# Performance work log

Hardware: AMD Instinct MI355X
Metric: run time of the kernel (lower is better)

The kernel has to match this reference:

```python
import jax, jax.numpy as jnp
import numpy as np

N_NODES = 10000
N_EDGES = 160000
D = 42          # node_input_dim == node_hidden_dim
DE = 10         # edge_input_dim
DEH = 42        # edge_hidden_dim
N_STEPS = 6


def setup_inputs() -> dict:
    key = jax.random.key(0)
    ks = jax.random.split(key, 16)
    s = 0.1
    return {
        "n_feat": jax.random.normal(ks[0], (N_NODES, D), jnp.float32),
        "e_feat": jax.random.normal(ks[1], (N_EDGES, DE), jnp.float32),
        "src": jax.random.randint(ks[2], (N_EDGES,), 0, N_NODES),
        "dst": jax.random.randint(ks[3], (N_EDGES,), 0, N_NODES),
        # lin0: node_input_dim -> node_hidden_dim
        "lin0_w": s * jax.random.normal(ks[4], (D, D), jnp.float32),
        "lin0_b": s * jax.random.normal(ks[5], (D,), jnp.float32),
        # message_layer: hidden -> hidden
        "msg_w": s * jax.random.normal(ks[6], (D, D), jnp.float32),
        "msg_b": s * jax.random.normal(ks[7], (D,), jnp.float32),
        # edge_network: Linear(10,42) -> ReLU -> Linear(42, 42*42)
        "en_w1": s * jax.random.normal(ks[8], (DE, DEH), jnp.float32),
        "en_b1": s * jax.random.normal(ks[9], (DEH,), jnp.float32),
        "en_w2": s * jax.random.normal(ks[10], (DEH, D * D), jnp.float32),
        "en_b2": s * jax.random.normal(ks[11], (D * D,), jnp.float32),
        # NNConv bias (DGL NNConv has bias=True by default)
        "conv_b": s * jax.random.normal(ks[12], (D,), jnp.float32),
    }


def reference(n_feat, e_feat, src, dst,
              lin0_w, lin0_b, msg_w, msg_b,
              en_w1, en_b1, en_w2, en_b2, conv_b):
    N, d = n_feat.shape
    init = n_feat
    out = jax.nn.relu(n_feat @ lin0_w + lin0_b)                      # [N, d]
    # Per-edge weight matrices from edge features (e_feat is constant
    # across steps, so the edge MLP is hoisted out of the loop).
    w_edge = (jax.nn.relu(e_feat @ en_w1 + en_b1) @ en_w2 + en_b2)   # [E, d*d]
    w_edge = w_edge.reshape(-1, d, d)                                # [E, d_in, d_out]
    for _ in range(N_STEPS):
        # NNConv: gather src feats, per-edge matvec, scatter-sum to dst
        msgs = jnp.einsum('ei,eio->eo', out[src], w_edge)            # [E, d]
        agg = jax.ops.segment_sum(msgs, dst, num_segments=N)         # [N, d]
        # residual (in==out -> identity res_fc) + bias, then outer ReLU
        m = jax.nn.relu(agg + out + conv_b)
        out = jax.nn.relu(m @ msg_w + msg_b)
    return out + init
```

## Files before the change

### kernel.cpp

```cpp
#include <hip/hip_runtime.h>
#include <hip/hip_bf16.h>


#define N_NODES 10000
#define N_EDGES 160000
#define NCHK 5000
#define D 42
#define DE 10
#define XSTR 48
#define KI 1806
#define NKSTEP 57
#define SSTR 1832

typedef __attribute__((ext_vector_type(8))) short short8;
typedef __attribute__((ext_vector_type(4))) float f32x4;

__global__ __launch_bounds__(256) void k_lin0(const float* __restrict__ nf,
        const float* __restrict__ w, const float* __restrict__ b,
        __hip_bfloat16* __restrict__ out16) {
    int idx = blockIdx.x * 256 + threadIdx.x;
    if (idx >= N_NODES * XSTR) return;
    int n = idx / XSTR, j = idx % XSTR;
    float v = 0.f;
    if (j < D) {
        const float* row = nf + n * D;
        float acc = b[j];
        #pragma unroll
        for (int i = 0; i < D; ++i) acc = fmaf(row[i], w[i * D + j], acc);
        v = fmaxf(acc, 0.f);
    }
    out16[idx] = __float2bfloat16(v);
}

__global__ __launch_bounds__(256) void k_T2B(const float* __restrict__ w2,
        const float* __restrict__ b2, __hip_bfloat16* __restrict__ Bfr) {
    int idx = blockIdx.x * 256 + threadIdx.x;
    if (idx >= 3 * NKSTEP * 64 * 8) return;
    int j = idx & 7, lane = (idx >> 3) & 63;
    int ks = (idx >> 9) % NKSTEP, nt = idx / (NKSTEP * 512);
    int col = nt * 16 + (lane & 15);
    int k = ks * 32 + ((lane >> 4) * 8) + j;
    float v = 0.f;
    if (col < D && k < KI) {
        int kk = k / D, ii = k % D;
        v = (kk < D) ? w2[kk * (D * D) + ii * D + col] : b2[ii * D + col];
    }
    Bfr[idx] = __float2bfloat16(v);
}

__global__ __launch_bounds__(256) void k_hist(const int* __restrict__ dst,
        int* __restrict__ cnt) {
    int e = blockIdx.x * 256 + threadIdx.x;
    if (e < N_EDGES) atomicAdd(&cnt[dst[e]], 1);
}

__global__ __launch_bounds__(1024) void k_scan(const int* __restrict__ cnt,
        int* __restrict__ row_ptr, int* __restrict__ cursor) {
    __shared__ int buf[1024];
    __shared__ int s_run;
    const int t = threadIdx.x;
    if (t == 0) s_run = 0;
    __syncthreads();
    for (int base = 0; base < N_NODES; base += 1024) {
        int v = (base + t < N_NODES) ? cnt[base + t] : 0;
        buf[t] = v;
        __syncthreads();
        for (int off = 1; off < 1024; off <<= 1) {
            int add = (t >= off) ? buf[t - off] : 0;
            __syncthreads();
            buf[t] += add;
            __syncthreads();
        }
        int excl = buf[t] - v;
        if (base + t < N_NODES) {
            int val = s_run + excl;
            row_ptr[base + t] = val;
            cursor[base + t]  = val;
        }
        __syncthreads();
        if (t == 0) s_run += buf[1023];
        __syncthreads();
    }
    if (t == 0) { row_ptr[N_NODES] = s_run; cursor[N_NODES] = s_run; }
}

__global__ __launch_bounds__(256) void k_scatter(const int* __restrict__ dst,
        const int* __restrict__ src, int* __restrict__ cursor,
        int* __restrict__ srcp, int* __restrict__ eperm) {
    int e = blockIdx.x * 256 + threadIdx.x;
    if (e < N_EDGES) {
        int p = atomicAdd(&cursor[dst[e]], 1);
        srcp[p] = src[e];
        eperm[p] = e;
    }
}

__global__ __launch_bounds__(256) void k_hT(const float* __restrict__ ef,
        const float* __restrict__ w1, const float* __restrict__ b1,
        const int* __restrict__ eperm, __hip_bfloat16* __restrict__ hpT) {
    const int c = blockIdx.x;
    const int t = threadIdx.x;
    for (int j = t; j < 48 * 32; j += 256) {
        int k = j >> 5, ep = j & 31;
        int e = eperm[c * 32 + ep];
        float v;
        if (k < D) {
            const float* row = ef + (size_t)e * DE;
            float acc = b1[k];
            #pragma unroll
            for (int i = 0; i < DE; ++i) acc = fmaf(row[i], w1[i * D + k], acc);
            v = fmaxf(acc, 0.f);
        } else {
            v = (k == D) ? 1.0f : 0.f;
        }
        hpT[(size_t)c * 1536 + j] = __float2bfloat16(v);
    }
}

#define MFMA(A, B, C) C = __builtin_amdgcn_mfma_f32_16x16x32_bf16(A, B, C, 0, 0, 0)

__global__ __launch_bounds__(512, 6) void k_step6(
        const __hip_bfloat16* __restrict__ hpT,
        const __hip_bfloat16* __restrict__ out_in,
        const int* __restrict__ srcp, const int* __restrict__ row_ptr,
        const __hip_bfloat16* __restrict__ Bfr,
        const float* __restrict__ nf, const float* __restrict__ msg_w,
        const float* __restrict__ msg_b, const float* __restrict__ conv_b,
        __hip_bfloat16* __restrict__ out16_dst, float* __restrict__ fout,
        int last) {
    __shared__ __align__(16) __hip_bfloat16 sS[8 * SSTR];
    __shared__ float sR[8 * 48];
    __shared__ float sM[8 * 48];
    const int t = threadIdx.x;
    const int wv = t >> 6;
    const int l = t & 63;
    const int g = l >> 4;
    const int g8 = g * 8;
    const int cl = l & 15;
    const int n0 = blockIdx.x * 8;
    const short* hpTs = (const short*)hpT;
    const short* xs = (const short*)out_in;

    for (int i = t; i < 8 * 48; i += 512) sR[i] = 0.f;
    for (int i = t; i < 8 * 18; i += 512)
        sS[(i / 18) * SSTR + KI + (i % 18)] = __float2bfloat16(0.f);

    {
        const int node = n0 + wv;
        const int beg = row_ptr[node], end = row_ptr[node + 1];
        const int c0 = beg >> 5;
        const int nc = (end > beg) ? ((end - 1) >> 5) - c0 + 1 : 0;

        f32x4 cc[9];
        #pragma unroll
        for (int i = 0; i < 9; ++i) cc[i] = {0.f, 0.f, 0.f, 0.f};

        for (int ci = 0; ci < nc; ++ci) {
            const int c = c0 + ci;
            const int c32 = c << 5;
            const size_t hb = (size_t)c * 1536 + cl * 32 + g8;
            short8 a0 = *(const short8*)(hpTs + hb);
            short8 a1 = *(const short8*)(hpTs + hb + 512);
            short8 a2 = *(const short8*)(hpTs + hb + 1024);
            if (c32 < beg || c32 + 32 > end) {
                #pragma unroll
                for (int j = 0; j < 8; ++j) {
                    int ep = c32 + g8 + j;
                    if (ep < beg || ep >= end) { a0[j] = 0; a1[j] = 0; a2[j] = 0; }
                }
            }
            int4 s0 = *(const int4*)(srcp + c32 + g8);
            int4 s1 = *(const int4*)(srcp + c32 + g8 + 4);
            const int se[8] = {s0.x, s0.y, s0.z, s0.w, s1.x, s1.y, s1.z, s1.w};
            #pragma unroll
            for (int nt = 0; nt < 3; ++nt) {
                short8 b;
                #pragma unroll
                for (int j = 0; j < 8; ++j)
                    b[j] = xs[(size_t)se[j] * XSTR + nt * 16 + cl];
                MFMA(a0, b, cc[0 * 3 + nt]);
                MFMA(a1, b, cc[1 * 3 + nt]);
                MFMA(a2, b, cc[2 * 3 + nt]);
            }
        }
        #define ST(CI, MT, NT)                                               \
            _Pragma("unroll")                                                \
            for (int r = 0; r < 4; ++r) {                                    \
                int m = (MT) * 16 + g * 4 + r;                               \
                int col = (NT) * 16 + cl;                                    \
                if (m < 43 && col < D)                                       \
                    sS[wv * SSTR + m * D + col] = __float2bfloat16(cc[CI][r]); \
            }
        ST(0, 0, 0) ST(1, 0, 1) ST(2, 0, 2)
        ST(3, 1, 0) ST(4, 1, 1) ST(5, 1, 2)
        ST(6, 2, 0) ST(7, 2, 1) ST(8, 2, 2)
        #undef ST
    }
    __syncthreads();

    {
        const int ks0 = (wv == 0) ? 0 : (wv * 7 + 1);
        const int ks1 = wv * 7 + 8;
        f32x4 d0 = {0.f, 0.f, 0.f, 0.f}, d1 = d0, d2 = d0;
        const short* sSrow = (const short*)sS + (cl & 7) * SSTR + g8;
        const short* bb = (const short*)Bfr + (size_t)l * 8;
        for (int ks = ks0; ks < ks1; ++ks) {
            short8 a  = *(const short8*)(sSrow + ks * 32);
            short8 B0 = *(const short8*)(bb + (size_t)(0 * NKSTEP + ks) * 512);
            short8 B1 = *(const short8*)(bb + (size_t)(1 * NKSTEP + ks) * 512);
            short8 B2 = *(const short8*)(bb + (size_t)(2 * NKSTEP + ks) * 512);
            MFMA(a, B0, d0); MFMA(a, B1, d1); MFMA(a, B2, d2);
        }
        if (g < 2) {
            const int rl = g * 4;
            #pragma unroll
            for (int r = 0; r < 4; ++r) {
                atomicAdd(&sR[(rl + r) * 48 + cl],      d0[r]);
                atomicAdd(&sR[(rl + r) * 48 + 16 + cl], d1[r]);
                atomicAdd(&sR[(rl + r) * 48 + 32 + cl], d2[r]);
            }
        }
    }
    __syncthreads();

    float* sW = (float*)sS;
    for (int i = t; i < D * D; i += 512) sW[i] = msg_w[i];
    for (int idx = t; idx < 8 * 48; idx += 512) {
        int nl_ = idx / 48, o = idx % 48;
        float mv = 0.f;
        if (o < D) {
            float res = __bfloat162float(out_in[(size_t)(n0 + nl_) * XSTR + o]);
            mv = fmaxf(sR[idx] + res + conv_b[o], 0.f);
        }
        sM[idx] = mv;
    }
    __syncthreads();

    for (int idx = t; idx < 8 * 48; idx += 512) {
        int nl_ = idx / 48, pcol = idx % 48;
        if (pcol < D) {
            float s = msg_b[pcol];
            #pragma unroll 6
            for (int o = 0; o < D; ++o)
                s = fmaf(sM[nl_ * 48 + o], sW[o * D + pcol], s);
            float v = fmaxf(s, 0.f);
            if (last) {
                fout[(size_t)(n0 + nl_) * D + pcol] =
                    v + nf[(size_t)(n0 + nl_) * D + pcol];
            } else {
                out16_dst[(size_t)(n0 + nl_) * XSTR + pcol] = __float2bfloat16(v);
            }
        } else if (!last) {
            out16_dst[(size_t)(n0 + nl_) * XSTR + pcol] = __float2bfloat16(0.f);
        }
    }
}

extern "C" void kernel_launch(void* const* d_in, const int* in_sizes, int n_in,
                              void* d_out, int out_size, void* d_ws, size_t ws_size,
                              hipStream_t stream) {
    const float* nf    = (const float*)d_in[0];
    const float* ef    = (const float*)d_in[1];
    const int*   src   = (const int*)d_in[2];
    const int*   dst   = (const int*)d_in[3];
    const float* lin0w = (const float*)d_in[4];
    const float* lin0b = (const float*)d_in[5];
    const float* msgw  = (const float*)d_in[6];
    const float* msgb  = (const float*)d_in[7];
    const float* enw1  = (const float*)d_in[8];
    const float* enb1  = (const float*)d_in[9];
    const float* enw2  = (const float*)d_in[10];
    const float* enb2  = (const float*)d_in[11];
    const float* convb = (const float*)d_in[12];

    char* p = (char*)d_ws;
    auto alloc = [&](size_t bytes) -> char* {
        char* r = p; p += (bytes + 255) & ~(size_t)255; return r;
    };
    __hip_bfloat16* outA = (__hip_bfloat16*)alloc((size_t)N_NODES * XSTR * 2);
    __hip_bfloat16* outB = (__hip_bfloat16*)alloc((size_t)N_NODES * XSTR * 2);
    __hip_bfloat16* hpT  = (__hip_bfloat16*)alloc((size_t)NCHK * 1536 * 2);
    __hip_bfloat16* Bfr  = (__hip_bfloat16*)alloc((size_t)3 * NKSTEP * 64 * 8 * 2);
    int* cnt    = (int*)alloc((N_NODES + 1) * 4);
    int* rowp   = (int*)alloc((N_NODES + 1) * 4);
    int* cur    = (int*)alloc((N_NODES + 1) * 4);
    int* srcp   = (int*)alloc((size_t)N_EDGES * 4);
    int* eperm  = (int*)alloc((size_t)N_EDGES * 4);

    hipMemsetAsync(cnt, 0, (N_NODES + 1) * 4, stream);
    k_lin0<<<(N_NODES * XSTR + 255) / 256, 256, 0, stream>>>(nf, lin0w, lin0b, outA);
    k_T2B<<<(3 * NKSTEP * 64 * 8 + 255) / 256, 256, 0, stream>>>(enw2, enb2, Bfr);
    k_hist<<<(N_EDGES + 255) / 256, 256, 0, stream>>>(dst, cnt);
    k_scan<<<1, 1024, 0, stream>>>(cnt, rowp, cur);
    k_scatter<<<(N_EDGES + 255) / 256, 256, 0, stream>>>(dst, src, cur, srcp, eperm);
    k_hT<<<NCHK, 256, 0, stream>>>(ef, enw1, enb1, eperm, hpT);

    const int tiles = N_NODES / 8;
    __hip_bfloat16* bufs[2] = {outA, outB};
    for (int s_i = 0; s_i < 6; ++s_i) {
        const __hip_bfloat16* cin = bufs[s_i % 2];
        __hip_bfloat16* cout = bufs[(s_i + 1) % 2];
        int last = (s_i == 5) ? 1 : 0;
        k_step6<<<tiles, 512, 0, stream>>>(hpT, cin, srcp, rowp, Bfr,
                                           nf, msgw, msgb, convb,
                                           cout, (float*)d_out, last);
    }
}
```

Measured before the change: 365.9 us.

## Fuse six step launches into one persistent cooperative kernel with grid sync

```diff
diff --git a/kernel.cpp b/kernel.cpp
--- a/kernel.cpp
+++ b/kernel.cpp
@@ -1,10 +1,14 @@
 #include <hip/hip_runtime.h>
 #include <hip/hip_bf16.h>
+#include <hip/hip_cooperative_groups.h>
+
+namespace cg = cooperative_groups;
 
 
 #define N_NODES 10000
 #define N_EDGES 160000
 #define NCHK 5000
+#define NTILES 1250
 #define D 42
 #define DE 10
 #define XSTR 48
@@ -119,139 +123,169 @@
 
 #define MFMA(A, B, C) C = __builtin_amdgcn_mfma_f32_16x16x32_bf16(A, B, C, 0, 0, 0)
 
-__global__ __launch_bounds__(512, 6) void k_step6(
+__global__ __launch_bounds__(512, 4) void k_persist(
         const __hip_bfloat16* __restrict__ hpT,
-        const __hip_bfloat16* __restrict__ out_in,
+        __hip_bfloat16* __restrict__ outA,
+        __hip_bfloat16* __restrict__ outB,
         const int* __restrict__ srcp, const int* __restrict__ row_ptr,
         const __hip_bfloat16* __restrict__ Bfr,
         const float* __restrict__ nf, const float* __restrict__ msg_w,
         const float* __restrict__ msg_b, const float* __restrict__ conv_b,
-        __hip_bfloat16* __restrict__ out16_dst, float* __restrict__ fout,
-        int last) {
+        float* __restrict__ fout, int* __restrict__ tilectr) {
     __shared__ __align__(16) __hip_bfloat16 sS[8 * SSTR];
+    __shared__ float sW[D * D];
     __shared__ float sR[8 * 48];
     __shared__ float sM[8 * 48];
+    __shared__ int s_tile;
+    cg::grid_group gg = cg::this_grid();
+
     const int t = threadIdx.x;
     const int wv = t >> 6;
     const int l = t & 63;
     const int g = l >> 4;
     const int g8 = g * 8;
     const int cl = l & 15;
-    const int n0 = blockIdx.x * 8;
     const short* hpTs = (const short*)hpT;
-    const short* xs = (const short*)out_in;
-
-    for (int i = t; i < 8 * 48; i += 512) sR[i] = 0.f;
+
     for (int i = t; i < 8 * 18; i += 512)
         sS[(i / 18) * SSTR + KI + (i % 18)] = __float2bfloat16(0.f);
-
-    {
-        const int node = n0 + wv;
-        const int beg = row_ptr[node], end = row_ptr[node + 1];
-        const int c0 = beg >> 5;
-        const int nc = (end > beg) ? ((end - 1) >> 5) - c0 + 1 : 0;
-
-        f32x4 cc[9];
-        #pragma unroll
-        for (int i = 0; i < 9; ++i) cc[i] = {0.f, 0.f, 0.f, 0.f};
-
-        for (int ci = 0; ci < nc; ++ci) {
-            const int c = c0 + ci;
-            const int c32 = c << 5;
-            const size_t hb = (size_t)c * 1536 + cl * 32 + g8;
-            short8 a0 = *(const short8*)(hpTs + hb);
-            short8 a1 = *(const short8*)(hpTs + hb + 512);
-            short8 a2 = *(const short8*)(hpTs + hb + 1024);
-            if (c32 < beg || c32 + 32 > end) {
+    for (int i = t; i < D * D; i += 512) sW[i] = msg_w[i];
+
+    for (int step = 0; step < 6; ++step) {
+        const __hip_bfloat16* cin = (step & 1) ? outB : outA;
+        __hip_bfloat16* cout = (step & 1) ? outA : outB;
+        const int last = (step == 5);
+        const short* xs = (const short*)cin;
+
+        for (;;) {
+            if (t == 0) s_tile = atomicAdd(&tilectr[step], 1);
+            __syncthreads();
+            const int tile = s_tile;
+            if (tile >= NTILES) break;
+            const int n0 = tile * 8;
+
+            for (int i = t; i < 8 * 48; i += 512) sR[i] = 0.f;
+
+            {
+                const int node = n0 + wv;
+                const int beg = row_ptr[node], end = row_ptr[node + 1];
+                const int c0 = beg >> 5;
+                const int nc = (end > beg) ? ((end - 1) >> 5) - c0 + 1 : 0;
+
+                f32x4 cc[9];
                 #pragma unroll
-                for (int j = 0; j < 8; ++j) {
-                    int ep = c32 + g8 + j;
-                    if (ep < beg || ep >= end) { a0[j] = 0; a1[j] = 0; a2[j] = 0; }
-                }
+                for (int i = 0; i < 9; ++i) cc[i] = {0.f, 0.f, 0.f, 0.f};
+
+                for (int ci = 0; ci < nc; ++ci) {
+                    const int c = c0 + ci;
+                    const int c32 = c << 5;
+                    const size_t hb = (size_t)c * 1536 + cl * 32 + g8;
+                    short8 a0 = *(const short8*)(hpTs + hb);
+                    short8 a1 = *(const short8*)(hpTs + hb + 512);
+                    short8 a2 = *(const short8*)(hpTs + hb + 1024);
+                    if (c32 < beg || c32 + 32 > end) {
+                        #pragma unroll
+                        for (int j = 0; j < 8; ++j) {
+                            int ep = c32 + g8 + j;
+                            if (ep < beg || ep >= end) {
+                                a0[j] = 0; a1[j] = 0; a2[j] = 0;
+                            }
+                        }
+                    }
+                    int4 s0 = *(const int4*)(srcp + c32 + g8);
+                    int4 s1 = *(const int4*)(srcp + c32 + g8 + 4);
+                    const int se[8] = {s0.x, s0.y, s0.z, s0.w,
+                                       s1.x, s1.y, s1.z, s1.w};
+                    #pragma unroll
+                    for (int nt = 0; nt < 3; ++nt) {
+                        short8 b;
+                        #pragma unroll
+                        for (int j = 0; j < 8; ++j)
+                            b[j] = xs[(size_t)se[j] * XSTR + nt * 16 + cl];
+                        MFMA(a0, b, cc[0 * 3 + nt]);
+                        MFMA(a1, b, cc[1 * 3 + nt]);
+                        MFMA(a2, b, cc[2 * 3 + nt]);
+                    }
+                }
+                #define ST(CI, MT, NT)                                       \
+                    _Pragma("unroll")                                        \
+                    for (int r = 0; r < 4; ++r) {                            \
+                        int m = (MT) * 16 + g * 4 + r;                       \
+                        int col = (NT) * 16 + cl;                            \
+                        if (m < 43 && col < D)                               \
+                            sS[wv * SSTR + m * D + col] =                    \
+                                __float2bfloat16(cc[CI][r]);                 \
+                    }
+                ST(0, 0, 0) ST(1, 0, 1) ST(2, 0, 2)
+                ST(3, 1, 0) ST(4, 1, 1) ST(5, 1, 2)
+                ST(6, 2, 0) ST(7, 2, 1) ST(8, 2, 2)
+                #undef ST
             }
-            int4 s0 = *(const int4*)(srcp + c32 + g8);
-            int4 s1 = *(const int4*)(srcp + c32 + g8 + 4);
-            const int se[8] = {s0.x, s0.y, s0.z, s0.w, s1.x, s1.y, s1.z, s1.w};
-            #pragma unroll
-            for (int nt = 0; nt < 3; ++nt) {
-                short8 b;
-                #pragma unroll
-                for (int j = 0; j < 8; ++j)
-                    b[j] = xs[(size_t)se[j] * XSTR + nt * 16 + cl];
-                MFMA(a0, b, cc[0 * 3 + nt]);
-                MFMA(a1, b, cc[1 * 3 + nt]);
-                MFMA(a2, b, cc[2 * 3 + nt]);
+            __syncthreads();
+
+            {
+                const int ks0 = (wv == 0) ? 0 : (wv * 7 + 1);
+                const int ks1 = wv * 7 + 8;
+                f32x4 d0 = {0.f, 0.f, 0.f, 0.f}, d1 = d0, d2 = d0;
+                const short* sSrow = (const short*)sS + (cl & 7) * SSTR + g8;
+                const short* bb = (const short*)Bfr + (size_t)l * 8;
+                for (int ks = ks0; ks < ks1; ++ks) {
+                    short8 a  = *(const short8*)(sSrow + ks * 32);
+                    short8 B0 = *(const short8*)(bb + (size_t)(0 * NKSTEP + ks) * 512);
+                    short8 B1 = *(const short8*)(bb + (size_t)(1 * NKSTEP + ks) * 512);
+                    short8 B2 = *(const short8*)(bb + (size_t)(2 * NKSTEP + ks) * 512);
+                    MFMA(a, B0, d0); MFMA(a, B1, d1); MFMA(a, B2, d2);
+                }
+                if (g < 2) {
+                    const int rl = g * 4;
+                    #pragma unroll
+                    for (int r = 0; r < 4; ++r) {
+                        atomicAdd(&sR[(rl + r) * 48 + cl],      d0[r]);
+                        atomicAdd(&sR[(rl + r) * 48 + 16 + cl], d1[r]);
+                        atomicAdd(&sR[(rl + r) * 48 + 32 + cl], d2[r]);
+                    }
+                }
             }
-        }
-        #define ST(CI, MT, NT)                                               \
-            _Pragma("unroll")                                                \
-            for (int r = 0; r < 4; ++r) {                                    \
-                int m = (MT) * 16 + g * 4 + r;                               \
-                int col = (NT) * 16 + cl;                                    \
-                if (m < 43 && col < D)                                       \
-                    sS[wv * SSTR + m * D + col] = __float2bfloat16(cc[CI][r]); \
+            __syncthreads();
+
+            for (int idx = t; idx < 8 * 48; idx += 512) {
+                int nl_ = idx / 48, o = idx % 48;
+                float mv = 0.f;
+                if (o < D) {
+                    float res = __bfloat162float(
+                        cin[(size_t)(n0 + nl_) * XSTR + o]);
+                    mv = fmaxf(sR[idx] + res + conv_b[o], 0.f);
+                }
+                sM[idx] = mv;
             }
-        ST(0, 0, 0) ST(1, 0, 1) ST(2, 0, 2)
-        ST(3, 1, 0) ST(4, 1, 1) ST(5, 1, 2)
-        ST(6, 2, 0) ST(7, 2, 1) ST(8, 2, 2)
-        #undef ST
-    }
-    __syncthreads();
-
-    {
-        const int ks0 = (wv == 0) ? 0 : (wv * 7 + 1);
-        const int ks1 = wv * 7 + 8;
-        f32x4 d0 = {0.f, 0.f, 0.f, 0.f}, d1 = d0, d2 = d0;
-        const short* sSrow = (const short*)sS + (cl & 7) * SSTR + g8;
-        const short* bb = (const short*)Bfr + (size_t)l * 8;
-        for (int ks = ks0; ks < ks1; ++ks) {
-            short8 a  = *(const short8*)(sSrow + ks * 32);
-            short8 B0 = *(const short8*)(bb + (size_t)(0 * NKSTEP + ks) * 512);
-            short8 B1 = *(const short8*)(bb + (size_t)(1 * NKSTEP + ks) * 512);
-            short8 B2 = *(const short8*)(bb + (size_t)(2 * NKSTEP + ks) * 512);
-            MFMA(a, B0, d0); MFMA(a, B1, d1); MFMA(a, B2, d2);
-        }
-        if (g < 2) {
-            const int rl = g * 4;
-            #pragma unroll
-            for (int r = 0; r < 4; ++r) {
-                atomicAdd(&sR[(rl + r) * 48 + cl],      d0[r]);
-                atomicAdd(&sR[(rl + r) * 48 + 16 + cl], d1[r]);
-                atomicAdd(&sR[(rl + r) * 48 + 32 + cl], d2[r]);
+            __syncthreads();
+
+            for (int idx = t; idx < 8 * 48; idx += 512) {
+                int nl_ = idx / 48, pcol = idx % 48;
+                if (pcol < D) {
+                    float s = msg_b[pcol];
+                    #pragma unroll 6
+                    for (int o = 0; o < D; ++o)
+                        s = fmaf(sM[nl_ * 48 + o], sW[o * D + pcol], s);
+                    float v = fmaxf(s, 0.f);
+                    if (last) {
+                        fout[(size_t)(n0 + nl_) * D + pcol] =
+                            v + nf[(size_t)(n0 + nl_) * D + pcol];
+                    } else {
+                        cout[(size_t)(n0 + nl_) * XSTR + pcol] =
+                            __float2bfloat16(v);
+                    }
+                } else if (!last) {
+                    cout[(size_t)(n0 + nl_) * XSTR + pcol] =
+                        __float2bfloat16(0.f);
+                }
             }
         }
-    }
-    __syncthreads();
-
-    float* sW = (float*)sS;
-    for (int i = t; i < D * D; i += 512) sW[i] = msg_w[i];
-    for (int idx = t; idx < 8 * 48; idx += 512) {
-        int nl_ = idx / 48, o = idx % 48;
-        float mv = 0.f;
-        if (o < D) {
-            float res = __bfloat162float(out_in[(size_t)(n0 + nl_) * XSTR + o]);
-            mv = fmaxf(sR[idx] + res + conv_b[o], 0.f);
-        }
-        sM[idx] = mv;
-    }
-    __syncthreads();
-
-    for (int idx = t; idx < 8 * 48; idx += 512) {
-        int nl_ = idx / 48, pcol = idx % 48;
-        if (pcol < D) {
-            float s = msg_b[pcol];
-            #pragma unroll 6
-            for (int o = 0; o < D; ++o)
-                s = fmaf(sM[nl_ * 48 + o], sW[o * D + pcol], s);
-            float v = fmaxf(s, 0.f);
-            if (last) {
-                fout[(size_t)(n0 + nl_) * D + pcol] =
-                    v + nf[(size_t)(n0 + nl_) * D + pcol];
-            } else {
-                out16_dst[(size_t)(n0 + nl_) * XSTR + pcol] = __float2bfloat16(v);
-            }
-        } else if (!last) {
-            out16_dst[(size_t)(n0 + nl_) * XSTR + pcol] = __float2bfloat16(0.f);
+
+        if (step < 5) {
+            __threadfence();
+            gg.sync();
+            __builtin_amdgcn_fence(__ATOMIC_ACQUIRE, "agent");
         }
     }
 }
@@ -286,8 +320,11 @@
     int* cur    = (int*)alloc((N_NODES + 1) * 4);
     int* srcp   = (int*)alloc((size_t)N_EDGES * 4);
     int* eperm  = (int*)alloc((size_t)N_EDGES * 4);
+    int* tilectr = (int*)alloc(8 * 4);
+    float* fo   = (float*)d_out;
 
     hipMemsetAsync(cnt, 0, (N_NODES + 1) * 4, stream);
+    hipMemsetAsync(tilectr, 0, 8 * 4, stream);
     k_lin0<<<(N_NODES * XSTR + 255) / 256, 256, 0, stream>>>(nf, lin0w, lin0b, outA);
     k_T2B<<<(3 * NKSTEP * 64 * 8 + 255) / 256, 256, 0, stream>>>(enw2, enb2, Bfr);
     k_hist<<<(N_EDGES + 255) / 256, 256, 0, stream>>>(dst, cnt);
@@ -295,14 +332,16 @@
     k_scatter<<<(N_EDGES + 255) / 256, 256, 0, stream>>>(dst, src, cur, srcp, eperm);
     k_hT<<<NCHK, 256, 0, stream>>>(ef, enw1, enb1, eperm, hpT);
 
-    const int tiles = N_NODES / 8;
-    __hip_bfloat16* bufs[2] = {outA, outB};
-    for (int s_i = 0; s_i < 6; ++s_i) {
-        const __hip_bfloat16* cin = bufs[s_i % 2];
-        __hip_bfloat16* cout = bufs[(s_i + 1) % 2];
-        int last = (s_i == 5) ? 1 : 0;
-        k_step6<<<tiles, 512, 0, stream>>>(hpT, cin, srcp, rowp, Bfr,
-                                           nf, msgw, msgb, convb,
-                                           cout, (float*)d_out, last);
-    }
-}
+    int maxb = 0;
+    hipOccupancyMaxActiveBlocksPerMultiprocessor(&maxb, k_persist, 512, 0);
+    if (maxb < 1) maxb = 1;
+    if (maxb > 4) maxb = 4;
+    int grid = maxb * 256;
+    if (grid > NTILES) grid = NTILES;
+
+    void* args[] = {(void*)&hpT, (void*)&outA, (void*)&outB, (void*)&srcp,
+                    (void*)&rowp, (void*)&Bfr, (void*)&nf, (void*)&msgw,
+                    (void*)&msgb, (void*)&convb, (void*)&fo, (void*)&tilectr};
+    hipLaunchCooperativeKernel(reinterpret_cast<void*>(k_persist),
+                               dim3(grid), dim3(512), args, 0, stream);
+}
```

After: 824.0 us. 125% more time.

## Stage gathered source features cooperatively in LDS windows and merge prep kernels

Applied to the files above, without the earlier changes.

```diff
diff --git a/kernel.cpp b/kernel.cpp
--- a/kernel.cpp
+++ b/kernel.cpp
@@ -11,33 +11,33 @@
 #define KI 1806
 #define NKSTEP 57
 #define SSTR 1832
+#define WCH 6
 
 typedef __attribute__((ext_vector_type(8))) short short8;
 typedef __attribute__((ext_vector_type(4))) float f32x4;
 
-__global__ __launch_bounds__(256) void k_lin0(const float* __restrict__ nf,
-        const float* __restrict__ w, const float* __restrict__ b,
-        __hip_bfloat16* __restrict__ out16) {
+__global__ __launch_bounds__(256) void k_prep(const float* __restrict__ nf,
+        const float* __restrict__ lw, const float* __restrict__ lb,
+        const float* __restrict__ w2, const float* __restrict__ b2,
+        __hip_bfloat16* __restrict__ out16, __hip_bfloat16* __restrict__ Bfr) {
     int idx = blockIdx.x * 256 + threadIdx.x;
-    if (idx >= N_NODES * XSTR) return;
-    int n = idx / XSTR, j = idx % XSTR;
-    float v = 0.f;
-    if (j < D) {
-        const float* row = nf + n * D;
-        float acc = b[j];
-        #pragma unroll
-        for (int i = 0; i < D; ++i) acc = fmaf(row[i], w[i * D + j], acc);
-        v = fmaxf(acc, 0.f);
-    }
-    out16[idx] = __float2bfloat16(v);
-}
-
-__global__ __launch_bounds__(256) void k_T2B(const float* __restrict__ w2,
-        const float* __restrict__ b2, __hip_bfloat16* __restrict__ Bfr) {
-    int idx = blockIdx.x * 256 + threadIdx.x;
-    if (idx >= 3 * NKSTEP * 64 * 8) return;
-    int j = idx & 7, lane = (idx >> 3) & 63;
-    int ks = (idx >> 9) % NKSTEP, nt = idx / (NKSTEP * 512);
+    if (idx < N_NODES * XSTR) {
+        int n = idx / XSTR, j = idx % XSTR;
+        float v = 0.f;
+        if (j < D) {
+            const float* row = nf + n * D;
+            float acc = lb[j];
+            #pragma unroll
+            for (int i = 0; i < D; ++i) acc = fmaf(row[i], lw[i * D + j], acc);
+            v = fmaxf(acc, 0.f);
+        }
+        out16[idx] = __float2bfloat16(v);
+        return;
+    }
+    int idx2 = idx - N_NODES * XSTR;
+    if (idx2 >= 3 * NKSTEP * 64 * 8) return;
+    int j = idx2 & 7, lane = (idx2 >> 3) & 63;
+    int ks = (idx2 >> 9) % NKSTEP, nt = idx2 / (NKSTEP * 512);
     int col = nt * 16 + (lane & 15);
     int k = ks * 32 + ((lane >> 4) * 8) + j;
     float v = 0.f;
@@ -45,7 +45,7 @@
         int kk = k / D, ii = k % D;
         v = (kk < D) ? w2[kk * (D * D) + ii * D + col] : b2[ii * D + col];
     }
-    Bfr[idx] = __float2bfloat16(v);
+    Bfr[idx2] = __float2bfloat16(v);
 }
 
 __global__ __launch_bounds__(256) void k_hist(const int* __restrict__ dst,
@@ -119,7 +119,7 @@
 
 #define MFMA(A, B, C) C = __builtin_amdgcn_mfma_f32_16x16x32_bf16(A, B, C, 0, 0, 0)
 
-__global__ __launch_bounds__(512, 6) void k_step6(
+__global__ __launch_bounds__(512, 4) void k_step9(
         const __hip_bfloat16* __restrict__ hpT,
         const __hip_bfloat16* __restrict__ out_in,
         const int* __restrict__ srcp, const int* __restrict__ row_ptr,
@@ -129,8 +129,10 @@
         __hip_bfloat16* __restrict__ out16_dst, float* __restrict__ fout,
         int last) {
     __shared__ __align__(16) __hip_bfloat16 sS[8 * SSTR];
+    __shared__ __align__(16) short xcT[WCH * 1536];
     __shared__ float sR[8 * 48];
     __shared__ float sM[8 * 48];
+    short* xc = (short*)sS;
     const int t = threadIdx.x;
     const int wv = t >> 6;
     const int l = t & 63;
@@ -142,21 +144,48 @@
     const short* xs = (const short*)out_in;
 
     for (int i = t; i < 8 * 48; i += 512) sR[i] = 0.f;
-    for (int i = t; i < 8 * 18; i += 512)
-        sS[(i / 18) * SSTR + KI + (i % 18)] = __float2bfloat16(0.f);
-
-    {
-        const int node = n0 + wv;
-        const int beg = row_ptr[node], end = row_ptr[node + 1];
-        const int c0 = beg >> 5;
-        const int nc = (end > beg) ? ((end - 1) >> 5) - c0 + 1 : 0;
-
-        f32x4 cc[9];
-        #pragma unroll
-        for (int i = 0; i < 9; ++i) cc[i] = {0.f, 0.f, 0.f, 0.f};
-
-        for (int ci = 0; ci < nc; ++ci) {
-            const int c = c0 + ci;
+
+    const int beg8 = row_ptr[n0], end8 = row_ptr[n0 + 8];
+    const int c0b = beg8 >> 5;
+    const int cspan = (end8 > beg8) ? ((end8 - 1) >> 5) - c0b + 1 : 0;
+    const int nwin = (cspan + WCH - 1) / WCH;
+
+    const int node = n0 + wv;
+    const int beg = row_ptr[node], end = row_ptr[node + 1];
+    const int c0n = beg >> 5;
+    const int cmaxn = (end > beg) ? ((end - 1) >> 5) : c0n - 1;
+
+    f32x4 cc[9];
+    #pragma unroll
+    for (int i = 0; i < 9; ++i) cc[i] = {0.f, 0.f, 0.f, 0.f};
+
+    for (int w = 0; w < nwin; ++w) {
+        const int cw0 = c0b + w * WCH;
+        if (w) __syncthreads();
+        for (int idx = t; idx < 192 * 6; idx += 512) {
+            int el = idx / 6, cs = idx - el * 6;
+            int p = (cw0 << 5) + el;
+            short8 v = {0, 0, 0, 0, 0, 0, 0, 0};
+            if (p < N_EDGES) {
+                int sp = srcp[p];
+                v = *(const short8*)(xs + (size_t)sp * XSTR + cs * 8);
+            }
+            *(short8*)&xc[el * 50 + cs * 8] = v;
+        }
+        __syncthreads();
+        for (int idx = t; idx < WCH * 192; idx += 512) {
+            int ccq = idx / 192, rem = idx - ccq * 192;
+            int row = rem >> 2, h8 = rem & 3;
+            short8 v;
+            #pragma unroll
+            for (int j = 0; j < 8; ++j)
+                v[j] = xc[(ccq * 32 + h8 * 8 + j) * 50 + row];
+            *(short8*)&xcT[ccq * 1536 + row * 32 + h8 * 8] = v;
+        }
+        __syncthreads();
+        const int clo = (c0n > cw0) ? c0n : cw0;
+        const int chi = (cmaxn < cw0 + WCH - 1) ? cmaxn : cw0 + WCH - 1;
+        for (int c = clo; c <= chi; ++c) {
             const int c32 = c << 5;
             const size_t hb = (size_t)c * 1536 + cl * 32 + g8;
             short8 a0 = *(const short8*)(hpTs + hb);
@@ -169,33 +198,28 @@
                     if (ep < beg || ep >= end) { a0[j] = 0; a1[j] = 0; a2[j] = 0; }
                 }
             }
-            int4 s0 = *(const int4*)(srcp + c32 + g8);
-            int4 s1 = *(const int4*)(srcp + c32 + g8 + 4);
-            const int se[8] = {s0.x, s0.y, s0.z, s0.w, s1.x, s1.y, s1.z, s1.w};
-            #pragma unroll
-            for (int nt = 0; nt < 3; ++nt) {
-                short8 b;
-                #pragma unroll
-                for (int j = 0; j < 8; ++j)
-                    b[j] = xs[(size_t)se[j] * XSTR + nt * 16 + cl];
-                MFMA(a0, b, cc[0 * 3 + nt]);
-                MFMA(a1, b, cc[1 * 3 + nt]);
-                MFMA(a2, b, cc[2 * 3 + nt]);
-            }
-        }
-        #define ST(CI, MT, NT)                                               \
-            _Pragma("unroll")                                                \
-            for (int r = 0; r < 4; ++r) {                                    \
-                int m = (MT) * 16 + g * 4 + r;                               \
-                int col = (NT) * 16 + cl;                                    \
-                if (m < 43 && col < D)                                       \
-                    sS[wv * SSTR + m * D + col] = __float2bfloat16(cc[CI][r]); \
-            }
-        ST(0, 0, 0) ST(1, 0, 1) ST(2, 0, 2)
-        ST(3, 1, 0) ST(4, 1, 1) ST(5, 1, 2)
-        ST(6, 2, 0) ST(7, 2, 1) ST(8, 2, 2)
-        #undef ST
-    }
+            const int xb = (c - cw0) * 1536 + cl * 32 + g8;
+            short8 b0 = *(const short8*)&xcT[xb];
+            short8 b1 = *(const short8*)&xcT[xb + 512];
+            short8 b2 = *(const short8*)&xcT[xb + 1024];
+            MFMA(a0, b0, cc[0]); MFMA(a0, b1, cc[1]); MFMA(a0, b2, cc[2]);
+            MFMA(a1, b0, cc[3]); MFMA(a1, b1, cc[4]); MFMA(a1, b2, cc[5]);
+            MFMA(a2, b0, cc[6]); MFMA(a2, b1, cc[7]); MFMA(a2, b2, cc[8]);
+        }
+    }
+    #define ST(CI, MT, NT)                                                   \
+        _Pragma("unroll")                                                    \
+        for (int r = 0; r < 4; ++r) {                                        \
+            int m = (MT) * 16 + g * 4 + r;                                   \
+            int col = (NT) * 16 + cl;                                        \
+            if (m < 43 && col < D)                                           \
+                sS[wv * SSTR + m * D + col] = __float2bfloat16(cc[CI][r]);   \
+        }
+    ST(0, 0, 0) ST(1, 0, 1) ST(2, 0, 2)
+    ST(3, 1, 0) ST(4, 1, 1) ST(5, 1, 2)
+    ST(6, 2, 0) ST(7, 2, 1) ST(8, 2, 2)
+    #undef ST
+    if (l < 18) sS[wv * SSTR + KI + l] = __float2bfloat16(0.f);
     __syncthreads();
 
     {
@@ -288,8 +312,9 @@
     int* eperm  = (int*)alloc((size_t)N_EDGES * 4);
 
     hipMemsetAsync(cnt, 0, (N_NODES + 1) * 4, stream);
-    k_lin0<<<(N_NODES * XSTR + 255) / 256, 256, 0, stream>>>(nf, lin0w, lin0b, outA);
-    k_T2B<<<(3 * NKSTEP * 64 * 8 + 255) / 256, 256, 0, stream>>>(enw2, enb2, Bfr);
+    const int prep_total = N_NODES * XSTR + 3 * NKSTEP * 64 * 8;
+    k_prep<<<(prep_total + 255) / 256, 256, 0, stream>>>(
+        nf, lin0w, lin0b, enw2, enb2, outA, Bfr);
     k_hist<<<(N_EDGES + 255) / 256, 256, 0, stream>>>(dst, cnt);
     k_scan<<<1, 1024, 0, stream>>>(cnt, rowp, cur);
     k_scatter<<<(N_EDGES + 255) / 256, 256, 0, stream>>>(dst, src, cur, srcp, eperm);
@@ -301,7 +326,7 @@
         const __hip_bfloat16* cin = bufs[s_i % 2];
         __hip_bfloat16* cout = bufs[(s_i + 1) % 2];
         int last = (s_i == 5) ? 1 : 0;
-        k_step6<<<tiles, 512, 0, stream>>>(hpT, cin, srcp, rowp, Bfr,
+        k_step9<<<tiles, 512, 0, stream>>>(hpT, cin, srcp, rowp, Bfr,
                                            nf, msgw, msgb, convb,
                                            cout, (float*)d_out, last);
     }
```

Result: slower. 374.9 us (+2.4%).
